# Kernel tuning notes

Measured on AMD Instinct MI355X. Metric: run time of the kernel, lower is better.

Reference implementation:

```python
import jax, jax.numpy as jnp
import numpy as np

BIT_WIDTH = 8
QMAX = 2.0 ** (BIT_WIDTH - 1) - 1  # 127
QMIN = -(2.0 ** (BIT_WIDTH - 1))   # -128


def fake_quant(x, reduce_axes):
    """Symmetric int8 fake-quantization with per-channel abs-max scale.
    reduce_axes: axes reduced to compute the per-channel scale (channel dims kept).
    """
    scale = jnp.max(jnp.abs(x), axis=reduce_axes, keepdims=True) / QMAX
    scale = jnp.maximum(scale, 1e-8)
    q = jnp.clip(jnp.round(x / scale), QMIN, QMAX)
    return q * scale


def setup_inputs() -> dict:
    key = jax.random.key(0)
    ks = jax.random.split(key, 7)
    B, T, D = 4, 2048, 512
    return {
        "query": jax.random.normal(ks[0], (B, T, D), dtype=jnp.float32),
        "key": jax.random.normal(ks[1], (B, T, D), dtype=jnp.float32),
        "value": jax.random.normal(ks[2], (B, T, D), dtype=jnp.float32),
        "Wq": jax.random.normal(ks[3], (D, D), dtype=jnp.float32),
        "Wk": jax.random.normal(ks[4], (D, D), dtype=jnp.float32),
        "Wv": jax.random.normal(ks[5], (D, D), dtype=jnp.float32),
        "Wf": jax.random.normal(ks[6], (D, D), dtype=jnp.float32),
    }


def reference(query, key, value, Wq, Wk, Wv, Wf):
    H = 8
    B, T, D = query.shape
    dk = D // H

    # Activation fake-quant: per-token scale (stats over batch and feature dims)
    qx = fake_quant(query, (0, 2))
    kx = fake_quant(key, (0, 2))
    vx = fake_quant(value, (0, 2))
    # Weight fake-quant: per output column scale (stats over input rows)
    wq = fake_quant(Wq, (0,))
    wk = fake_quant(Wk, (0,))
    wv = fake_quant(Wv, (0,))

    def proj(x, w):  # [B,T,D] @ [D,D] -> [B,H,T,dk]
        return (x @ w).reshape(B, T, H, dk).transpose(0, 2, 1, 3)

    q = proj(qx, wq)
    k = proj(kx, wk)
    v = proj(vx, wv)

    scores = jnp.einsum("bhqd,bhkd->bhqk", q, k) / jnp.sqrt(jnp.float32(dk))
    p_attn = jax.nn.softmax(scores, axis=-1)  # dropout omitted (eval mode)
    x = jnp.einsum("bhqk,bhkd->bhqd", p_attn, v)
    x = x.transpose(0, 2, 1, 3).reshape(B, T, D)

    # Output activation quantized; weights_final is NOT quantized in the original forward
    out = fake_quant(x, (0, 2)) @ Wf
    return out
```

## Files before the change

kernel.cpp:

```cpp
#include <hip/hip_runtime.h>
#include <math.h>


typedef _Float16 f16x8 __attribute__((ext_vector_type(8)));
typedef float f32x4 __attribute__((ext_vector_type(4)));
#define MFMA16(a, b, c) __builtin_amdgcn_mfma_f32_16x16x32_f16((a), (b), (c), 0, 0, 0)

__global__ __launch_bounds__(256) void token_scale(
    const float* __restrict__ x0, const float* __restrict__ x1,
    const float* __restrict__ x2, double* __restrict__ out)
{
    const int t = blockIdx.x;
    const int z = blockIdx.y;
    const float* __restrict__ x = (z == 0) ? x0 : ((z == 1) ? x1 : x2);
    const int tid = threadIdx.x;
    float m = 0.0f;
#pragma unroll
    for (int i = 0; i < 2; ++i) {
        int f = i * 256 + tid;
        int b = f >> 7, d4 = f & 127;
        float4 v = *(const float4*)(x + (long)(b * 2048 + t) * 512 + d4 * 4);
        m = fmaxf(m, fmaxf(fmaxf(fabsf(v.x), fabsf(v.y)), fmaxf(fabsf(v.z), fabsf(v.w))));
    }
#pragma unroll
    for (int off = 1; off < 64; off <<= 1) m = fmaxf(m, __shfl_xor(m, off));
    __shared__ float red[4];
    if ((tid & 63) == 0) red[tid >> 6] = m;
    __syncthreads();
    if (tid == 0) {
        m = fmaxf(fmaxf(red[0], red[1]), fmaxf(red[2], red[3]));
        out[z * 2048 + t] = fmax((double)m / 127.0, 1e-8);
    }
}

__global__ __launch_bounds__(256) void wquant(
    const float* __restrict__ Wq, const float* __restrict__ Wk,
    const float* __restrict__ Wv, double* __restrict__ sw,
    _Float16* __restrict__ qW)
{
    const int z = blockIdx.y;
    const float* __restrict__ W = (z == 0) ? Wq : (z == 1) ? Wk : Wv;
    const int col0 = blockIdx.x * 64;
    const int tid = threadIdx.x;
    const int c = tid & 63, kg = tid >> 6;

    __shared__ float redm[4][64];
    __shared__ double sS[64];
    __shared__ __align__(16) _Float16 qs[64][520];

    float m = 0.0f;
    for (int k = kg; k < 512; k += 4)
        m = fmaxf(m, fabsf(W[k * 512 + col0 + c]));
    redm[kg][c] = m;
    __syncthreads();
    if (tid < 64) {
        float mm = fmaxf(fmaxf(redm[0][tid], redm[1][tid]),
                         fmaxf(redm[2][tid], redm[3][tid]));
        double s = fmax((double)mm / 127.0, 1e-8);
        sw[z * 512 + col0 + tid] = s;
        sS[tid] = s;
    }
    __syncthreads();

    const double s = sS[c];
    for (int k = kg; k < 512; k += 4)
        qs[c][k] = (_Float16)fmin(fmax(rint((double)W[k * 512 + col0 + c] / s), -128.0), 127.0);
    __syncthreads();

    const int wc = tid >> 2, kc = (tid & 3) * 128;
    _Float16* q = qW + (long)z * 262144 + (long)(col0 + wc) * 512 + kc;
#pragma unroll
    for (int j = 0; j < 16; ++j)
        *(f16x8*)(q + j * 8) = *(const f16x8*)(&qs[wc][kc + j * 8]);
}

__global__ __launch_bounds__(256) void aquant(
    const float* __restrict__ x0, const float* __restrict__ x1,
    const float* __restrict__ x2, const double* __restrict__ sAll,
    _Float16* __restrict__ qA)
{
    const int z = blockIdx.y;
    const float* __restrict__ x = (z == 0) ? x0 : ((z == 1) ? x1 : x2);
    const double* __restrict__ s = sAll + z * 2048;
    const long PLANE = (long)4 * 2048 * 512;
    const long f = ((long)blockIdx.x * 256 + threadIdx.x) * 8;
    float4 v0 = *(const float4*)(x + f);
    float4 v1 = *(const float4*)(x + f + 4);
    const double sc = s[(f >> 9) & 2047];
    f16x8 q;
    q[0] = (_Float16)fmin(fmax(rint((double)v0.x / sc), -128.0), 127.0);
    q[1] = (_Float16)fmin(fmax(rint((double)v0.y / sc), -128.0), 127.0);
    q[2] = (_Float16)fmin(fmax(rint((double)v0.z / sc), -128.0), 127.0);
    q[3] = (_Float16)fmin(fmax(rint((double)v0.w / sc), -128.0), 127.0);
    q[4] = (_Float16)fmin(fmax(rint((double)v1.x / sc), -128.0), 127.0);
    q[5] = (_Float16)fmin(fmax(rint((double)v1.y / sc), -128.0), 127.0);
    q[6] = (_Float16)fmin(fmax(rint((double)v1.z / sc), -128.0), 127.0);
    q[7] = (_Float16)fmin(fmax(rint((double)v1.w / sc), -128.0), 127.0);
    *(f16x8*)(qA + (long)z * PLANE + f) = q;
}

__global__ __launch_bounds__(256) void wfsplit(
    const float* __restrict__ Wf, _Float16* __restrict__ WhT,
    _Float16* __restrict__ WlT)
{
    const int n0 = blockIdx.x * 64, k0 = blockIdx.y * 64;
    const int tid = threadIdx.x;
    __shared__ float T[64 * 68];
    {
        const int kr = tid >> 2, nc = (tid & 3) * 16;
#pragma unroll
        for (int j = 0; j < 4; ++j) {
            float4 v = *(const float4*)(Wf + (long)(k0 + kr) * 512 + n0 + nc + 4 * j);
            T[kr * 68 + nc + 4 * j + 0] = v.x;
            T[kr * 68 + nc + 4 * j + 1] = v.y;
            T[kr * 68 + nc + 4 * j + 2] = v.z;
            T[kr * 68 + nc + 4 * j + 3] = v.w;
        }
    }
    __syncthreads();
    const int nr = tid >> 2, kc = (tid & 3) * 16;
    f16x8 h[2], l[2];
#pragma unroll
    for (int j = 0; j < 16; ++j) {
        float wv = T[(kc + j) * 68 + nr];
        _Float16 hi = (_Float16)wv;
        h[j >> 3][j & 7] = hi;
        l[j >> 3][j & 7] = (_Float16)(wv - (float)hi);
    }
    *(f16x8*)(WhT + (long)(n0 + nr) * 512 + k0 + kc) = h[0];
    *(f16x8*)(WhT + (long)(n0 + nr) * 512 + k0 + kc + 8) = h[1];
    *(f16x8*)(WlT + (long)(n0 + nr) * 512 + k0 + kc) = l[0];
    *(f16x8*)(WlT + (long)(n0 + nr) * 512 + k0 + kc + 8) = l[1];
}

__global__ __launch_bounds__(256) void proj_mfma(
    const _Float16* __restrict__ qA, const _Float16* __restrict__ qW,
    const double* __restrict__ saAll, const double* __restrict__ swAll,
    _Float16* __restrict__ Qh, _Float16* __restrict__ Ql,
    _Float16* __restrict__ Kh, _Float16* __restrict__ Kl,
    _Float16* __restrict__ Vh, _Float16* __restrict__ Vl,
    int b)
{
    const int z = blockIdx.z;
    const _Float16* __restrict__ A = qA + ((long)z * 4 + b) * (2048l * 512);
    const _Float16* __restrict__ Bq = qW + (long)z * 262144;
    const double* __restrict__ sa = saAll + z * 2048;
    const double* __restrict__ swz = swAll + z * 512;

    const int m0 = blockIdx.x * 64, n0 = blockIdx.y * 64;
    const int tid = threadIdx.x;
    const int w = tid >> 6, lane = tid & 63;
    const int ln = lane & 15, quad = lane >> 4;

    __shared__ __align__(16) _Float16 As[64 * 72];
    __shared__ __align__(16) _Float16 Bs[64 * 72];
    const int srow = tid >> 3, scs = (tid & 7) * 8;

    f32x4 c[4];
#pragma unroll
    for (int nt = 0; nt < 4; ++nt) { c[nt][0] = 0; c[nt][1] = 0; c[nt][2] = 0; c[nt][3] = 0; }

    f16x8 a0, a1, b0, b1;
    a0 = *(const f16x8*)(A + (long)(m0 + srow) * 512 + scs);
    a1 = *(const f16x8*)(A + (long)(m0 + 32 + srow) * 512 + scs);
    b0 = *(const f16x8*)(Bq + (long)(n0 + srow) * 512 + scs);
    b1 = *(const f16x8*)(Bq + (long)(n0 + 32 + srow) * 512 + scs);

    for (int k0 = 0; k0 < 512; k0 += 64) {
        __syncthreads();
        *(f16x8*)(As + srow * 72 + scs) = a0;
        *(f16x8*)(As + (32 + srow) * 72 + scs) = a1;
        *(f16x8*)(Bs + srow * 72 + scs) = b0;
        *(f16x8*)(Bs + (32 + srow) * 72 + scs) = b1;
        __syncthreads();
        if (k0 + 64 < 512) {
            a0 = *(const f16x8*)(A + (long)(m0 + srow) * 512 + k0 + 64 + scs);
            a1 = *(const f16x8*)(A + (long)(m0 + 32 + srow) * 512 + k0 + 64 + scs);
            b0 = *(const f16x8*)(Bq + (long)(n0 + srow) * 512 + k0 + 64 + scs);
            b1 = *(const f16x8*)(Bq + (long)(n0 + 32 + srow) * 512 + k0 + 64 + scs);
        }
#pragma unroll
        for (int ks = 0; ks < 2; ++ks) {
            f16x8 aF = *(const f16x8*)(As + (w * 16 + ln) * 72 + ks * 32 + quad * 8);
#pragma unroll
            for (int nt = 0; nt < 4; ++nt) {
                f16x8 bF = *(const f16x8*)(Bs + (nt * 16 + ln) * 72 + ks * 32 + quad * 8);
                c[nt] = MFMA16(aF, bF, c[nt]);
            }
        }
    }

#pragma unroll
    for (int nt = 0; nt < 4; ++nt)
#pragma unroll
        for (int r = 0; r < 4; ++r) {
            int t = m0 + w * 16 + quad * 4 + r;
            int n = n0 + nt * 16 + ln;
            float val = (float)((double)c[nt][r] * sa[t] * swz[n]);
            _Float16 hi = (_Float16)val;
            _Float16 lo = (_Float16)(val - (float)hi);
            int hh = n >> 6, d = n & 63;
            if (z == 2) {
                long idx = ((long)hh * 64 + d) * 2048 + t;
                Vh[idx] = hi; Vl[idx] = lo;
            } else if (z == 1) {
                long idx = ((long)hh * 2048 + t) * 64 + d;
                Kh[idx] = hi; Kl[idx] = lo;
            } else {
                long idx = ((long)hh * 2048 + t) * 64 + d;
                Qh[idx] = hi; Ql[idx] = lo;
            }
        }
}

__global__ __launch_bounds__(256) void attn_mfma(
    const _Float16* __restrict__ Qh0, const _Float16* __restrict__ Ql0,
    const _Float16* __restrict__ Kh0, const _Float16* __restrict__ Kl0,
    const _Float16* __restrict__ Vh0, const _Float16* __restrict__ Vl0,
    float* __restrict__ xbuf, int bbase)
{
    const int q0 = blockIdx.x * 64;
    const int h = blockIdx.y;
    const int slot = blockIdx.z;
    const int b = bbase + slot;
    const long PE = (long)8 * 2048 * 64;
    const _Float16* __restrict__ Qh = Qh0 + (long)slot * PE;
    const _Float16* __restrict__ Ql = Ql0 + (long)slot * PE;
    const _Float16* __restrict__ Kh = Kh0 + (long)slot * PE;
    const _Float16* __restrict__ Kl = Kl0 + (long)slot * PE;
    const _Float16* __restrict__ Vh = Vh0 + (long)slot * PE;
    const _Float16* __restrict__ Vl = Vl0 + (long)slot * PE;

    const int tid = threadIdx.x;
    const int w = tid >> 6, lane = tid & 63;
    const int ln = lane & 15, quad = lane >> 4;

    __shared__ __align__(16) _Float16 KsH[64 * 72];
    __shared__ __align__(16) _Float16 KsL[64 * 72];
    __shared__ __align__(16) _Float16 VsH[64 * 72];
    __shared__ __align__(16) _Float16 VsL[64 * 72];
    __shared__ __align__(16) float SP[64 * 68];
    __shared__ float mS[64], lS[64], aS[64];
    __shared__ float psums[64 * 4];

    f16x8 qh[2], ql[2];
    {
        const long r = ((long)h * 2048 + q0 + w * 16 + ln) * 64 + quad * 8;
        qh[0] = *(const f16x8*)(Qh + r);
        qh[1] = *(const f16x8*)(Qh + r + 32);
        ql[0] = *(const f16x8*)(Ql + r);
        ql[1] = *(const f16x8*)(Ql + r + 32);
    }
    if (tid < 64) { mS[tid] = -INFINITY; lS[tid] = 0.0f; }

    f32x4 O[4];
#pragma unroll
    for (int dt = 0; dt < 4; ++dt) { O[dt][0] = 0; O[dt][1] = 0; O[dt][2] = 0; O[dt][3] = 0; }

    const int srow = tid >> 3, scs = (tid & 7) * 8;
    const long kBase = (long)h * 2048;
    const long vBase = (long)h * 64;
    f16x8 sg0, sg1, sg2, sg3, sg4, sg5, sg6, sg7;
    sg0 = *(const f16x8*)(Kh + (kBase + 0 + srow) * 64 + scs);
    sg1 = *(const f16x8*)(Kh + (kBase + 0 + 32 + srow) * 64 + scs);
    sg2 = *(const f16x8*)(Kl + (kBase + 0 + srow) * 64 + scs);
    sg3 = *(const f16x8*)(Kl + (kBase + 0 + 32 + srow) * 64 + scs);
    sg4 = *(const f16x8*)(Vh + (vBase + srow) * 2048 + 0 + scs);
    sg5 = *(const f16x8*)(Vh + (vBase + 32 + srow) * 2048 + 0 + scs);
    sg6 = *(const f16x8*)(Vl + (vBase + srow) * 2048 + 0 + scs);
    sg7 = *(const f16x8*)(Vl + (vBase + 32 + srow) * 2048 + 0 + scs);

    for (int k0 = 0; k0 < 2048; k0 += 64) {
        __syncthreads();
        *(f16x8*)(KsH + srow * 72 + scs)        = sg0;
        *(f16x8*)(KsH + (32 + srow) * 72 + scs) = sg1;
        *(f16x8*)(KsL + srow * 72 + scs)        = sg2;
        *(f16x8*)(KsL + (32 + srow) * 72 + scs) = sg3;
        *(f16x8*)(VsH + srow * 72 + scs)        = sg4;
        *(f16x8*)(VsH + (32 + srow) * 72 + scs) = sg5;
        *(f16x8*)(VsL + srow * 72 + scs)        = sg6;
        *(f16x8*)(VsL + (32 + srow) * 72 + scs) = sg7;
        __syncthreads();
        if (k0 + 64 < 2048) {
            const int kn = k0 + 64;
            sg0 = *(const f16x8*)(Kh + (kBase + kn + srow) * 64 + scs);
            sg1 = *(const f16x8*)(Kh + (kBase + kn + 32 + srow) * 64 + scs);
            sg2 = *(const f16x8*)(Kl + (kBase + kn + srow) * 64 + scs);
            sg3 = *(const f16x8*)(Kl + (kBase + kn + 32 + srow) * 64 + scs);
            sg4 = *(const f16x8*)(Vh + (vBase + srow) * 2048 + kn + scs);
            sg5 = *(const f16x8*)(Vh + (vBase + 32 + srow) * 2048 + kn + scs);
            sg6 = *(const f16x8*)(Vl + (vBase + srow) * 2048 + kn + scs);
            sg7 = *(const f16x8*)(Vl + (vBase + 32 + srow) * 2048 + kn + scs);
        }

#pragma unroll
        for (int kt = 0; kt < 4; ++kt) {
            f32x4 s; s[0] = 0; s[1] = 0; s[2] = 0; s[3] = 0;
#pragma unroll
            for (int ks = 0; ks < 2; ++ks) {
                const int off = (kt * 16 + ln) * 72 + ks * 32 + quad * 8;
                f16x8 bh = *(const f16x8*)(KsH + off);
                f16x8 bl = *(const f16x8*)(KsL + off);
                s = MFMA16(ql[ks], bh, s);
                s = MFMA16(qh[ks], bl, s);
                s = MFMA16(qh[ks], bh, s);
            }
#pragma unroll
            for (int r = 0; r < 4; ++r)
                SP[(w * 16 + quad * 4 + r) * 68 + kt * 16 + ln] = s[r] * 0.125f;
        }
        __syncthreads();

        {
            const int row = tid >> 2, c = tid & 3;
            const float* sp = SP + row * 68 + c;
            float rm = -INFINITY;
#pragma unroll
            for (int j = 0; j < 16; ++j) rm = fmaxf(rm, sp[4 * j]);
            rm = fmaxf(rm, __shfl_xor(rm, 1));
            rm = fmaxf(rm, __shfl_xor(rm, 2));
            if (c == 0) {
                float mold = mS[row];
                float mn = fmaxf(mold, rm);
                aS[row] = __expf(mold - mn);
                mS[row] = mn;
            }
        }
        __syncthreads();

        {
            const int row = tid >> 2, c = tid & 3;
            const float mn = mS[row];
            float* sp = SP + row * 68 + c;
            float sum = 0.0f;
#pragma unroll
            for (int j = 0; j < 16; ++j) {
                float p = __expf(sp[4 * j] - mn);
                sum += p;
                sp[4 * j] = p * 512.0f;
            }
            psums[row * 4 + c] = sum;
        }
#pragma unroll
        for (int r = 0; r < 4; ++r) {
            const float a = aS[w * 16 + quad * 4 + r];
#pragma unroll
            for (int dt = 0; dt < 4; ++dt) O[dt][r] *= a;
        }
        __syncthreads();

        if (tid < 64)
            lS[tid] = lS[tid] * aS[tid] +
                      (psums[tid * 4 + 0] + psums[tid * 4 + 1] +
                       psums[tid * 4 + 2] + psums[tid * 4 + 3]);

#pragma unroll
        for (int ks2 = 0; ks2 < 2; ++ks2) {
            const float* pp = SP + (w * 16 + ln) * 68 + ks2 * 32 + quad * 8;
            f16x8 ph, pl;
#pragma unroll
            for (int j = 0; j < 8; ++j) {
                float p = pp[j];
                _Float16 hi = (_Float16)p;
                ph[j] = hi;
                pl[j] = (_Float16)(p - (float)hi);
            }
#pragma unroll
            for (int dt = 0; dt < 4; ++dt) {
                const int off = (dt * 16 + ln) * 72 + ks2 * 32 + quad * 8;
                f16x8 vh = *(const f16x8*)(VsH + off);
                f16x8 vl = *(const f16x8*)(VsL + off);
                O[dt] = MFMA16(pl, vh, O[dt]);
                O[dt] = MFMA16(ph, vl, O[dt]);
                O[dt] = MFMA16(ph, vh, O[dt]);
            }
        }
    }

    __syncthreads();
#pragma unroll
    for (int r = 0; r < 4; ++r) {
        const int row = w * 16 + quad * 4 + r;
        const float inv = 1.0f / (512.0f * lS[row]);
        const long base = ((long)(b * 2048 + q0 + row)) * 512 + h * 64;
#pragma unroll
        for (int dt = 0; dt < 4; ++dt)
            xbuf[base + dt * 16 + ln] = O[dt][r] * inv;
    }
}

__global__ __launch_bounds__(256) void final_mfma(
    const _Float16* __restrict__ qX, const _Float16* __restrict__ WhT,
    const _Float16* __restrict__ WlT, const double* __restrict__ sx,
    float* __restrict__ out)
{
    const int m0 = blockIdx.x * 64, n0 = blockIdx.y * 64;
    const int tid = threadIdx.x;
    const int w = tid >> 6, lane = tid & 63;
    const int ln = lane & 15, quad = lane >> 4;

    __shared__ __align__(16) _Float16 As[64 * 72];
    __shared__ __align__(16) _Float16 BhS[64 * 72];
    __shared__ __align__(16) _Float16 BlS[64 * 72];
    const int srow = tid >> 3, scs = (tid & 7) * 8;

    f32x4 c[4];
#pragma unroll
    for (int nt = 0; nt < 4; ++nt) { c[nt][0] = 0; c[nt][1] = 0; c[nt][2] = 0; c[nt][3] = 0; }

    f16x8 a0, a1, h0, h1, l0, l1;
    a0 = *(const f16x8*)(qX + (long)(m0 + srow) * 512 + scs);
    a1 = *(const f16x8*)(qX + (long)(m0 + 32 + srow) * 512 + scs);
    h0 = *(const f16x8*)(WhT + (long)(n0 + srow) * 512 + scs);
    h1 = *(const f16x8*)(WhT + (long)(n0 + 32 + srow) * 512 + scs);
    l0 = *(const f16x8*)(WlT + (long)(n0 + srow) * 512 + scs);
    l1 = *(const f16x8*)(WlT + (long)(n0 + 32 + srow) * 512 + scs);

    for (int k0 = 0; k0 < 512; k0 += 64) {
        __syncthreads();
        *(f16x8*)(As + srow * 72 + scs) = a0;
        *(f16x8*)(As + (32 + srow) * 72 + scs) = a1;
        *(f16x8*)(BhS + srow * 72 + scs) = h0;
        *(f16x8*)(BhS + (32 + srow) * 72 + scs) = h1;
        *(f16x8*)(BlS + srow * 72 + scs) = l0;
        *(f16x8*)(BlS + (32 + srow) * 72 + scs) = l1;
        __syncthreads();
        if (k0 + 64 < 512) {
            a0 = *(const f16x8*)(qX + (long)(m0 + srow) * 512 + k0 + 64 + scs);
            a1 = *(const f16x8*)(qX + (long)(m0 + 32 + srow) * 512 + k0 + 64 + scs);
            h0 = *(const f16x8*)(WhT + (long)(n0 + srow) * 512 + k0 + 64 + scs);
            h1 = *(const f16x8*)(WhT + (long)(n0 + 32 + srow) * 512 + k0 + 64 + scs);
            l0 = *(const f16x8*)(WlT + (long)(n0 + srow) * 512 + k0 + 64 + scs);
            l1 = *(const f16x8*)(WlT + (long)(n0 + 32 + srow) * 512 + k0 + 64 + scs);
        }
#pragma unroll
        for (int ks = 0; ks < 2; ++ks) {
            f16x8 aF = *(const f16x8*)(As + (w * 16 + ln) * 72 + ks * 32 + quad * 8);
#pragma unroll
            for (int nt = 0; nt < 4; ++nt) {
                const int off = (nt * 16 + ln) * 72 + ks * 32 + quad * 8;
                f16x8 bh = *(const f16x8*)(BhS + off);
                f16x8 bl = *(const f16x8*)(BlS + off);
                c[nt] = MFMA16(aF, bl, c[nt]);
                c[nt] = MFMA16(aF, bh, c[nt]);
            }
        }
    }

#pragma unroll
    for (int nt = 0; nt < 4; ++nt)
#pragma unroll
        for (int r = 0; r < 4; ++r) {
            int m = m0 + w * 16 + quad * 4 + r;
            int n = n0 + nt * 16 + ln;
            out[(long)m * 512 + n] = (float)((double)c[nt][r] * sx[m & 2047]);
        }
}

extern "C" void kernel_launch(void* const* d_in, const int* in_sizes, int n_in,
                              void* d_out, int out_size, void* d_ws, size_t ws_size,
                              hipStream_t stream)
{
    const float* query = (const float*)d_in[0];
    const float* key_  = (const float*)d_in[1];
    const float* value = (const float*)d_in[2];
    const float* Wq = (const float*)d_in[3];
    const float* Wk = (const float*)d_in[4];
    const float* Wv = (const float*)d_in[5];
    const float* Wf = (const float*)d_in[6];
    float* out = (float*)d_out;

    char* p = (char*)d_ws;
    auto alloc = [&](size_t bytes) -> char* {
        char* r = p;
        p += (bytes + 255) & ~(size_t)255;
        return r;
    };
    double*   sA   = (double*)alloc(3 * 2048 * 8);
    double*   sx   = (double*)alloc(2048 * 8);
    double*   sw   = (double*)alloc(3 * 512 * 8);
    _Float16* qW   = (_Float16*)alloc((size_t)3 * 512 * 512 * 2);
    const long PE  = (long)8 * 2048 * 64;
    _Float16* Qh   = (_Float16*)alloc((size_t)2 * PE * 2);
    _Float16* Ql   = (_Float16*)alloc((size_t)2 * PE * 2);
    _Float16* Kh   = (_Float16*)alloc((size_t)2 * PE * 2);
    _Float16* Kl   = (_Float16*)alloc((size_t)2 * PE * 2);
    _Float16* Vh   = (_Float16*)alloc((size_t)2 * PE * 2);
    _Float16* Vl   = (_Float16*)alloc((size_t)2 * PE * 2);
    float*    xbuf = (float*)alloc((size_t)8192 * 512 * 4);
    _Float16* qA   = (_Float16*)alloc((size_t)3 * 4 * 2048 * 512 * 2);
    _Float16* WhT  = (_Float16*)alloc((size_t)512 * 512 * 2);
    _Float16* WlT  = (_Float16*)alloc((size_t)512 * 512 * 2);

    token_scale<<<dim3(2048, 3), 256, 0, stream>>>(query, key_, value, sA);
    wquant<<<dim3(8, 3), 256, 0, stream>>>(Wq, Wk, Wv, sw, qW);
    aquant<<<dim3(2048, 3), 256, 0, stream>>>(query, key_, value, sA, qA);
    wfsplit<<<dim3(8, 8), 256, 0, stream>>>(Wf, WhT, WlT);
    for (int pair = 0; pair < 2; ++pair) {
        proj_mfma<<<dim3(32, 8, 3), 256, 0, stream>>>(qA, qW, sA, sw,
            Qh, Ql, Kh, Kl, Vh, Vl, pair * 2);
        proj_mfma<<<dim3(32, 8, 3), 256, 0, stream>>>(qA, qW, sA, sw,
            Qh + PE, Ql + PE, Kh + PE, Kl + PE, Vh + PE, Vl + PE, pair * 2 + 1);
        attn_mfma<<<dim3(32, 8, 2), 256, 0, stream>>>(Qh, Ql, Kh, Kl, Vh, Vl, xbuf, pair * 2);
    }
    token_scale<<<dim3(2048, 1), 256, 0, stream>>>(xbuf, xbuf, xbuf, sx);
    aquant<<<dim3(2048, 1), 256, 0, stream>>>(xbuf, xbuf, xbuf, sx, qA);
    final_mfma<<<dim3(128, 8), 256, 0, stream>>>(qA, WhT, WlT, sx, out);
}
```

Before: 441.6 us.

## Compute attention softmax in registers via transposed MFMA, drop shared-memory score round trips

The MFMA operands are swapped so each lane holds a full column of scores for one query row. This lets row max and row sum be done with register reductions and two cross-lane shuffles instead of a shared score buffer and several block barriers. Probabilities are split into fp16 hi/lo and written to a per-wave shared tile for the PV MFMA, which only needs wave-local ordering. The output is then written with float4 stores. This removes three __syncthreads per key tile and the float shared traffic, at the cost of relying on wave-level sync for the per-wave P tile.

```diff
diff --git a/kernel.cpp b/kernel.cpp
--- a/kernel.cpp
+++ b/kernel.cpp
@@ -3,6 +3,7 @@
 
 
 typedef _Float16 f16x8 __attribute__((ext_vector_type(8)));
+typedef _Float16 f16x2 __attribute__((ext_vector_type(2)));
 typedef float f32x4 __attribute__((ext_vector_type(4)));
 #define MFMA16(a, b, c) __builtin_amdgcn_mfma_f32_16x16x32_f16((a), (b), (c), 0, 0, 0)
 
@@ -239,9 +240,8 @@
     __shared__ __align__(16) _Float16 KsL[64 * 72];
     __shared__ __align__(16) _Float16 VsH[64 * 72];
     __shared__ __align__(16) _Float16 VsL[64 * 72];
-    __shared__ __align__(16) float SP[64 * 68];
-    __shared__ float mS[64], lS[64], aS[64];
-    __shared__ float psums[64 * 4];
+    __shared__ __align__(16) _Float16 PTh[4][16 * 72];
+    __shared__ __align__(16) _Float16 PTl[4][16 * 72];
 
     f16x8 qh[2], ql[2];
     {
@@ -251,7 +251,8 @@
         ql[0] = *(const f16x8*)(Ql + r);
         ql[1] = *(const f16x8*)(Ql + r + 32);
     }
-    if (tid < 64) { mS[tid] = -INFINITY; lS[tid] = 0.0f; }
+
+    float m_run = -INFINITY, l_run = 0.0f;
 
     f32x4 O[4];
 #pragma unroll
@@ -293,99 +294,83 @@
             sg7 = *(const f16x8*)(Vl + (vBase + 32 + srow) * 2048 + kn + scs);
         }
 
+        f32x4 sT[4];
 #pragma unroll
         for (int kt = 0; kt < 4; ++kt) {
             f32x4 s; s[0] = 0; s[1] = 0; s[2] = 0; s[3] = 0;
 #pragma unroll
             for (int ks = 0; ks < 2; ++ks) {
                 const int off = (kt * 16 + ln) * 72 + ks * 32 + quad * 8;
-                f16x8 bh = *(const f16x8*)(KsH + off);
-                f16x8 bl = *(const f16x8*)(KsL + off);
-                s = MFMA16(ql[ks], bh, s);
-                s = MFMA16(qh[ks], bl, s);
-                s = MFMA16(qh[ks], bh, s);
-            }
-#pragma unroll
-            for (int r = 0; r < 4; ++r)
-                SP[(w * 16 + quad * 4 + r) * 68 + kt * 16 + ln] = s[r] * 0.125f;
-        }
-        __syncthreads();
-
-        {
-            const int row = tid >> 2, c = tid & 3;
-            const float* sp = SP + row * 68 + c;
-            float rm = -INFINITY;
-#pragma unroll
-            for (int j = 0; j < 16; ++j) rm = fmaxf(rm, sp[4 * j]);
-            rm = fmaxf(rm, __shfl_xor(rm, 1));
-            rm = fmaxf(rm, __shfl_xor(rm, 2));
-            if (c == 0) {
-                float mold = mS[row];
-                float mn = fmaxf(mold, rm);
-                aS[row] = __expf(mold - mn);
-                mS[row] = mn;
-            }
-        }
-        __syncthreads();
-
-        {
-            const int row = tid >> 2, c = tid & 3;
-            const float mn = mS[row];
-            float* sp = SP + row * 68 + c;
-            float sum = 0.0f;
-#pragma unroll
-            for (int j = 0; j < 16; ++j) {
-                float p = __expf(sp[4 * j] - mn);
-                sum += p;
-                sp[4 * j] = p * 512.0f;
-            }
-            psums[row * 4 + c] = sum;
-        }
-#pragma unroll
-        for (int r = 0; r < 4; ++r) {
-            const float a = aS[w * 16 + quad * 4 + r];
-#pragma unroll
-            for (int dt = 0; dt < 4; ++dt) O[dt][r] *= a;
-        }
-        __syncthreads();
-
-        if (tid < 64)
-            lS[tid] = lS[tid] * aS[tid] +
-                      (psums[tid * 4 + 0] + psums[tid * 4 + 1] +
-                       psums[tid * 4 + 2] + psums[tid * 4 + 3]);
+                f16x8 kh = *(const f16x8*)(KsH + off);
+                f16x8 kl = *(const f16x8*)(KsL + off);
+                s = MFMA16(kl, qh[ks], s);
+                s = MFMA16(kh, ql[ks], s);
+                s = MFMA16(kh, qh[ks], s);
+            }
+            sT[kt] = s;
+        }
+
+        float rm = -INFINITY;
+#pragma unroll
+        for (int kt = 0; kt < 4; ++kt)
+#pragma unroll
+            for (int r = 0; r < 4; ++r) rm = fmaxf(rm, sT[kt][r]);
+        rm = fmaxf(rm, __shfl_xor(rm, 16));
+        rm = fmaxf(rm, __shfl_xor(rm, 32));
+        const float mn = fmaxf(m_run, rm);
+        const float a = __expf((m_run - mn) * 0.125f);
+        m_run = mn;
+
+        float sum = 0.0f;
+#pragma unroll
+        for (int kt = 0; kt < 4; ++kt) {
+#pragma unroll
+            for (int r = 0; r < 4; r += 2) {
+                float p0 = __expf((sT[kt][r]     - mn) * 0.125f);
+                float p1 = __expf((sT[kt][r + 1] - mn) * 0.125f);
+                sum += p0 + p1;
+                float s0 = p0 * 512.0f, s1 = p1 * 512.0f;
+                _Float16 h0 = (_Float16)s0, h1 = (_Float16)s1;
+                f16x2 hp = {h0, h1};
+                f16x2 lp = {(_Float16)(s0 - (float)h0), (_Float16)(s1 - (float)h1)};
+                const int poff = ln * 72 + kt * 16 + quad * 4 + r;
+                *(f16x2*)(&PTh[w][poff]) = hp;
+                *(f16x2*)(&PTl[w][poff]) = lp;
+            }
+        }
+        sum += __shfl_xor(sum, 16);
+        sum += __shfl_xor(sum, 32);
+        l_run = l_run * a + sum;
+
+#pragma unroll
+        for (int dt = 0; dt < 4; ++dt) {
+            O[dt][0] *= a; O[dt][1] *= a; O[dt][2] *= a; O[dt][3] *= a;
+        }
 
 #pragma unroll
         for (int ks2 = 0; ks2 < 2; ++ks2) {
-            const float* pp = SP + (w * 16 + ln) * 68 + ks2 * 32 + quad * 8;
-            f16x8 ph, pl;
-#pragma unroll
-            for (int j = 0; j < 8; ++j) {
-                float p = pp[j];
-                _Float16 hi = (_Float16)p;
-                ph[j] = hi;
-                pl[j] = (_Float16)(p - (float)hi);
-            }
+            f16x8 ph = *(const f16x8*)(&PTh[w][ln * 72 + ks2 * 32 + quad * 8]);
+            f16x8 pl = *(const f16x8*)(&PTl[w][ln * 72 + ks2 * 32 + quad * 8]);
 #pragma unroll
             for (int dt = 0; dt < 4; ++dt) {
                 const int off = (dt * 16 + ln) * 72 + ks2 * 32 + quad * 8;
                 f16x8 vh = *(const f16x8*)(VsH + off);
                 f16x8 vl = *(const f16x8*)(VsL + off);
-                O[dt] = MFMA16(pl, vh, O[dt]);
-                O[dt] = MFMA16(ph, vl, O[dt]);
-                O[dt] = MFMA16(ph, vh, O[dt]);
-            }
-        }
-    }
-
-    __syncthreads();
-#pragma unroll
-    for (int r = 0; r < 4; ++r) {
-        const int row = w * 16 + quad * 4 + r;
-        const float inv = 1.0f / (512.0f * lS[row]);
-        const long base = ((long)(b * 2048 + q0 + row)) * 512 + h * 64;
-#pragma unroll
-        for (int dt = 0; dt < 4; ++dt)
-            xbuf[base + dt * 16 + ln] = O[dt][r] * inv;
+                O[dt] = MFMA16(vh, pl, O[dt]);
+                O[dt] = MFMA16(vl, ph, O[dt]);
+                O[dt] = MFMA16(vh, ph, O[dt]);
+            }
+        }
+    }
+
+    const float inv = 1.0f / (512.0f * l_run);
+    const long base = ((long)(b * 2048 + q0 + w * 16 + ln)) * 512 + h * 64 + quad * 4;
+#pragma unroll
+    for (int dt = 0; dt < 4; ++dt) {
+        float4 o;
+        o.x = O[dt][0] * inv; o.y = O[dt][1] * inv;
+        o.z = O[dt][2] * inv; o.w = O[dt][3] * inv;
+        *(float4*)(xbuf + base + dt * 16) = o;
     }
 }
 
```

New measurement: 423.6 us. -4.1%, faster.
